# Optimization experiments

Hardware: AMD Instinct MI355X
Metric: run time of the kernel (lower is better)

The kernel has to match this reference:

```python
import jax, jax.numpy as jnp
import numpy as np

B, N_IN, D_IN = 2048, 49, 320
D = 768            # inner_dim
H = 8              # n_heads
DH = D // H        # head dim = 96
NQ = 8             # n_queries
D_OUT = 3072       # llama_hidden
EPS = 1e-5


def _ln(x, g, b):
    mu = jnp.mean(x, axis=-1, keepdims=True)
    var = jnp.mean(jnp.square(x - mu), axis=-1, keepdims=True)
    return (x - mu) * jax.lax.rsqrt(var + EPS) * g + b


def setup_inputs() -> dict:
    key = jax.random.key(0)
    ks = jax.random.split(key, 16)
    s = lambda k, shape, fan: jax.random.normal(k, shape, jnp.float32) * (1.0 / np.sqrt(fan))
    return {
        "features": jax.random.normal(ks[0], (B, N_IN, D_IN), jnp.float32),
        "input_proj_w": s(ks[1], (D, D_IN), D_IN),
        "input_proj_b": jnp.zeros((D,), jnp.float32),
        "queries": jax.random.normal(ks[2], (NQ, D), jnp.float32) * 0.02,
        "ln_q_g": jnp.ones((D,), jnp.float32), "ln_q_b": jnp.zeros((D,), jnp.float32),
        "ln_kv_g": jnp.ones((D,), jnp.float32), "ln_kv_b": jnp.zeros((D,), jnp.float32),
        "in_proj_w": s(ks[3], (3 * D, D), D),
        "in_proj_b": jnp.zeros((3 * D,), jnp.float32),
        "out_proj_w": s(ks[4], (D, D), D),
        "out_proj_b": jnp.zeros((D,), jnp.float32),
        "ln_ff_g": jnp.ones((D,), jnp.float32), "ln_ff_b": jnp.zeros((D,), jnp.float32),
        "ffn_w1": s(ks[5], (D, D), D), "ffn_b1": jnp.zeros((D,), jnp.float32),
        "ffn_w2": s(ks[6], (D, D), D), "ffn_b2": jnp.zeros((D,), jnp.float32),
        "output_proj_w": s(ks[7], (D_OUT, D), D),
        "output_proj_b": jnp.zeros((D_OUT,), jnp.float32),
        "final_g": jnp.ones((D_OUT,), jnp.float32), "final_b": jnp.zeros((D_OUT,), jnp.float32),
    }


def reference(features, input_proj_w, input_proj_b, queries,
              ln_q_g, ln_q_b, ln_kv_g, ln_kv_b,
              in_proj_w, in_proj_b, out_proj_w, out_proj_b,
              ln_ff_g, ln_ff_b, ffn_w1, ffn_b1, ffn_w2, ffn_b2,
              output_proj_w, output_proj_b, final_g, final_b):
    b = features.shape[0]
    # kv projection: (B, N_in, D)
    kv = jnp.einsum('bnd,ed->bne', features, input_proj_w) + input_proj_b
    q = jnp.broadcast_to(queries[None], (b, NQ, D))

    # --- single layer (n_layers=1) ---
    q_norm = _ln(q, ln_q_g, ln_q_b)
    kv_norm = _ln(kv, ln_kv_g, ln_kv_b)

    wq, wk, wv = in_proj_w[:D], in_proj_w[D:2 * D], in_proj_w[2 * D:]
    bq, bk, bv = in_proj_b[:D], in_proj_b[D:2 * D], in_proj_b[2 * D:]
    qp = (jnp.einsum('bqd,ed->bqe', q_norm, wq) + bq).reshape(b, NQ, H, DH)
    kp = (jnp.einsum('bnd,ed->bne', kv_norm, wk) + bk).reshape(b, N_IN, H, DH)
    vp = (jnp.einsum('bnd,ed->bne', kv_norm, wv) + bv).reshape(b, N_IN, H, DH)

    scores = jnp.einsum('bqhd,bnhd->bhqn', qp, kp) / np.sqrt(DH).astype(np.float32)
    attn = jax.nn.softmax(scores, axis=-1)
    ctx = jnp.einsum('bhqn,bnhd->bqhd', attn, vp).reshape(b, NQ, D)
    attn_out = jnp.einsum('bqd,ed->bqe', ctx, out_proj_w) + out_proj_b

    q = q + attn_out
    h = _ln(q, ln_ff_g, ln_ff_b)
    h = jnp.einsum('bqd,ed->bqe', h, ffn_w1) + ffn_b1
    h = jax.nn.gelu(h, approximate=False)
    h = jnp.einsum('bqd,ed->bqe', h, ffn_w2) + ffn_b2
    q = q + h

    out = jnp.einsum('bqd,ed->bqe', q, output_proj_w) + output_proj_b
    return _ln(out, final_g, final_b)
```

## Files before the change

kernel.cpp:

```cpp
#include <hip/hip_runtime.h>
#include <math.h>

typedef __attribute__((ext_vector_type(8))) short short8;
typedef __attribute__((ext_vector_type(8))) unsigned short ushort8;
typedef __attribute__((ext_vector_type(4))) float f32x4;

__device__ __forceinline__ float b2f(unsigned short h) {
    union { unsigned int u; float f; } c; c.u = ((unsigned int)h) << 16; return c.f;
}
__device__ __forceinline__ unsigned short f2b(float x) {
    union { float f; unsigned int u; } c; c.f = x;
    unsigned int r = c.u + 0x7fffu + ((c.u >> 16) & 1u);
    return (unsigned short)(r >> 16);
}

__global__ __launch_bounds__(256) void cast_f2b(const float* __restrict__ in,
                                                unsigned short* __restrict__ out, int n4) {
    int i = blockIdx.x * 256 + threadIdx.x;
    if (i >= n4) return;
    float4 f = ((const float4*)in)[i];
    ushort4 o; o.x = f2b(f.x); o.y = f2b(f.y); o.z = f2b(f.z); o.w = f2b(f.w);
    ((ushort4*)out)[i] = o;
}

template <int DD, bool INB, bool OUTB>
__global__ __launch_bounds__(256) void ln_rows(const void* __restrict__ in_, void* __restrict__ out_,
                                               const float* __restrict__ g, const float* __restrict__ bb,
                                               int nrows) {
    const int wv = threadIdx.x >> 6, l = threadIdx.x & 63;
    const int row = blockIdx.x * 4 + wv;
    if (row >= nrows) return;
    constexpr int NC = DD / 256;
    float v[DD / 64];
    if constexpr (INB) {
        const ushort4* in = (const ushort4*)((const unsigned short*)in_ + (size_t)row * DD);
#pragma unroll
        for (int c = 0; c < NC; ++c) {
            ushort4 u = in[l + 64 * c];
            v[4*c] = b2f(u.x); v[4*c+1] = b2f(u.y); v[4*c+2] = b2f(u.z); v[4*c+3] = b2f(u.w);
        }
    } else {
        const float4* in = (const float4*)((const float*)in_ + (size_t)row * DD);
#pragma unroll
        for (int c = 0; c < NC; ++c) {
            float4 u = in[l + 64 * c];
            v[4*c] = u.x; v[4*c+1] = u.y; v[4*c+2] = u.z; v[4*c+3] = u.w;
        }
    }
    float s = 0.f, s2 = 0.f;
#pragma unroll
    for (int i = 0; i < DD / 64; ++i) { s += v[i]; s2 += v[i] * v[i]; }
#pragma unroll
    for (int o = 32; o > 0; o >>= 1) { s += __shfl_xor(s, o, 64); s2 += __shfl_xor(s2, o, 64); }
    const float mu = s * (1.0f / DD);
    const float var = s2 * (1.0f / DD) - mu * mu;
    const float rs = rsqrtf(var + 1e-5f);
    if constexpr (OUTB) {
        ushort4* out = (ushort4*)((unsigned short*)out_ + (size_t)row * DD);
#pragma unroll
        for (int c = 0; c < NC; ++c) {
            int e = (l + 64 * c) * 4;
            ushort4 o4;
            o4.x = f2b((v[4*c]   - mu) * rs * g[e]   + bb[e]);
            o4.y = f2b((v[4*c+1] - mu) * rs * g[e+1] + bb[e+1]);
            o4.z = f2b((v[4*c+2] - mu) * rs * g[e+2] + bb[e+2]);
            o4.w = f2b((v[4*c+3] - mu) * rs * g[e+3] + bb[e+3]);
            out[l + 64 * c] = o4;
        }
    } else {
        float4* out = (float4*)((float*)out_ + (size_t)row * DD);
#pragma unroll
        for (int c = 0; c < NC; ++c) {
            int e = (l + 64 * c) * 4;
            float4 o4;
            o4.x = (v[4*c]   - mu) * rs * g[e]   + bb[e];
            o4.y = (v[4*c+1] - mu) * rs * g[e+1] + bb[e+1];
            o4.z = (v[4*c+2] - mu) * rs * g[e+2] + bb[e+2];
            o4.w = (v[4*c+3] - mu) * rs * g[e+3] + bb[e+3];
            out[l + 64 * c] = o4;
        }
    }
}

__global__ __launch_bounds__(256) void qp_kernel(const float* __restrict__ qn, const float* __restrict__ wq,
                                                 const float* __restrict__ bq, float* __restrict__ qp) {
    int q = blockIdx.x / 3;
    int col = (blockIdx.x % 3) * 256 + threadIdx.x;
    const float4* a = (const float4*)(qn + q * 768);
    const float4* wr = (const float4*)(wq + (size_t)col * 768);
    float s = 0.f;
#pragma unroll 8
    for (int k = 0; k < 192; ++k) {
        float4 xx = a[k], yy = wr[k];
        s += xx.x * yy.x + xx.y * yy.y + xx.z * yy.z + xx.w * yy.w;
    }
    qp[q * 768 + col] = s + bq[col];
}

__global__ __launch_bounds__(256) void qk_build(const float* __restrict__ qp, const float* __restrict__ wk,
                                                unsigned short* __restrict__ qk) {
    const int hq = blockIdx.x, h = hq >> 3, q = hq & 7;
    const float* qv = qp + q * 768 + h * 96;
#pragma unroll
    for (int c = 0; c < 3; ++c) {
        int e = threadIdx.x + 256 * c;
        float s = 0.f;
        for (int d = 0; d < 96; ++d) s += qv[d] * wk[(size_t)(h * 96 + d) * 768 + e];
        qk[hq * 768 + e] = f2b(s * 0.10206207262f);
    }
}

__device__ __forceinline__ void gll16(const void* g, void* l) {
    __builtin_amdgcn_global_load_lds((const __attribute__((address_space(1))) unsigned int*)g,
                                     (__attribute__((address_space(3))) unsigned int*)l, 16, 0, 0);
}

template <int ROWS>
__device__ __forceinline__ void stage_rows(const unsigned short* gbase, int ldg,
                                           unsigned short* lds, int tid) {
    int wuni = tid & ~63;
#pragma unroll
    for (int it = 0; it < ROWS / 32; ++it) {
        int s = it * 256 + tid;
        int r = s >> 3, c = s & 7;
        int cc = c ^ (r & 7);
        gll16(gbase + (size_t)r * ldg + cc * 8, lds + (size_t)(it * 256 + wuni) * 8);
    }
}

template <int EPI>
__global__ __launch_bounds__(256) void gemm_bf16(
    const unsigned short* __restrict__ A, const unsigned short* __restrict__ W,
    const float* __restrict__ bias, void* __restrict__ out,
    const float* __restrict__ aux, int K, int N) {
    __shared__ __align__(16) unsigned short lA[128 * 64];
    __shared__ __align__(16) unsigned short lB[128 * 64];
    const int tid = threadIdx.x;
    const int l = tid & 63, w = tid >> 6;
    int gx = gridDim.x;
    int lid = blockIdx.y * gx + blockIdx.x;
    int nwg = gx * gridDim.y;
    int idx = (nwg & 7) ? lid : ((lid & 7) * (nwg >> 3) + (lid >> 3));
    const int bm0 = (idx / gx) * 128, bn0 = (idx % gx) * 128;
    const int wm = (w >> 1) * 64, wn = (w & 1) * 64;
    const int l15 = l & 15, lk = l >> 4;
    f32x4 acc[4][4] = {};
    const int nk = K >> 6;
    const unsigned short* Abase = A + (size_t)bm0 * K;
    const unsigned short* Wbase = W + (size_t)bn0 * K;
    for (int kt = 0; kt < nk; ++kt) {
        stage_rows<128>(Abase + kt * 64, K, lA, tid);
        stage_rows<128>(Wbase + kt * 64, K, lB, tid);
        __syncthreads();
        short8 af[4], bf[4];
#pragma unroll
        for (int kk = 0; kk < 2; ++kk) {
#pragma unroll
            for (int mf = 0; mf < 4; ++mf) {
                int r = wm + mf * 16 + l15;
                int c = (kk * 4 + lk) ^ (r & 7);
                af[mf] = *(const short8*)(lA + r * 64 + c * 8);
            }
#pragma unroll
            for (int nf = 0; nf < 4; ++nf) {
                int r = wn + nf * 16 + l15;
                int c = (kk * 4 + lk) ^ (r & 7);
                bf[nf] = *(const short8*)(lB + r * 64 + c * 8);
            }
#pragma unroll
            for (int mf = 0; mf < 4; ++mf)
#pragma unroll
                for (int nf = 0; nf < 4; ++nf)
                    acc[mf][nf] = __builtin_amdgcn_mfma_f32_16x16x32_bf16(af[mf], bf[nf], acc[mf][nf], 0, 0, 0);
        }
        __syncthreads();
    }
    const int row0 = bm0 + wm + (lk << 2);
    const int col0 = bn0 + wn + l15;
#pragma unroll
    for (int nf = 0; nf < 4; ++nf) {
        int col = col0 + nf * 16;
        float bv = bias[col];
#pragma unroll
        for (int mf = 0; mf < 4; ++mf) {
#pragma unroll
            for (int r = 0; r < 4; ++r) {
                int row = row0 + mf * 16 + r;
                float v = acc[mf][nf][r] + bv;
                size_t idx2 = (size_t)row * N + col;
                if constexpr (EPI == 0) {
                    ((unsigned short*)out)[idx2] = f2b(v);
                } else if constexpr (EPI == 1) {
                    v += aux[(row & 7) * N + col];
                    ((float*)out)[idx2] = v;
                } else if constexpr (EPI == 2) {
                    v = 0.5f * v * (1.0f + erff(v * 0.70710678118f));
                    ((unsigned short*)out)[idx2] = f2b(v);
                } else if constexpr (EPI == 3) {
                    v += aux[idx2];
                    ((unsigned short*)out)[idx2] = f2b(v);
                } else {
                    ((float*)out)[idx2] = v;
                }
            }
        }
    }
}

__global__ __launch_bounds__(256) void gemm_scores(const unsigned short* __restrict__ A,
                                                   const unsigned short* __restrict__ Qk,
                                                   float* __restrict__ S) {
    __shared__ __align__(16) unsigned short lA[128 * 64];
    __shared__ __align__(16) unsigned short lB[64 * 64];
    const int tid = threadIdx.x;
    const int l = tid & 63, w = tid >> 6;
    int lid = blockIdx.x;
    int idx = (lid & 7) * (gridDim.x >> 3) + (lid >> 3);
    const int bm0 = idx * 128;
    const int wm = (w >> 1) * 64, wn = (w & 1) * 32;
    const int l15 = l & 15, lk = l >> 4;
    f32x4 acc[4][2] = {};
    const unsigned short* Abase = A + (size_t)bm0 * 768;
    for (int kt = 0; kt < 12; ++kt) {
        stage_rows<128>(Abase + kt * 64, 768, lA, tid);
        stage_rows<64>(Qk + kt * 64, 768, lB, tid);
        __syncthreads();
        short8 af[4], bf[2];
#pragma unroll
        for (int kk = 0; kk < 2; ++kk) {
#pragma unroll
            for (int mf = 0; mf < 4; ++mf) {
                int r = wm + mf * 16 + l15;
                int c = (kk * 4 + lk) ^ (r & 7);
                af[mf] = *(const short8*)(lA + r * 64 + c * 8);
            }
#pragma unroll
            for (int nf = 0; nf < 2; ++nf) {
                int r = wn + nf * 16 + l15;
                int c = (kk * 4 + lk) ^ (r & 7);
                bf[nf] = *(const short8*)(lB + r * 64 + c * 8);
            }
#pragma unroll
            for (int mf = 0; mf < 4; ++mf)
#pragma unroll
                for (int nf = 0; nf < 2; ++nf)
                    acc[mf][nf] = __builtin_amdgcn_mfma_f32_16x16x32_bf16(af[mf], bf[nf], acc[mf][nf], 0, 0, 0);
        }
        __syncthreads();
    }
    const int row0 = bm0 + wm + (lk << 2);
    const int col0 = wn + l15;
#pragma unroll
    for (int nf = 0; nf < 2; ++nf)
#pragma unroll
        for (int mf = 0; mf < 4; ++mf)
#pragma unroll
            for (int r = 0; r < 4; ++r)
                S[(size_t)(row0 + mf * 16 + r) * 64 + col0 + nf * 16] = acc[mf][nf][r];
}

__global__ __launch_bounds__(256) void attn_mix(const unsigned short* __restrict__ kvn,
                                                const float* __restrict__ S,
                                                unsigned short* __restrict__ cmix) {
    __shared__ __align__(16) unsigned short at[64 * 64];
    __shared__ __align__(16) unsigned short kvT[384 * 64];
    float* Sl = (float*)kvT;
    const int b = blockIdx.x;
    const int t = threadIdx.x, l = t & 63, w = t >> 6;
    const int l15 = l & 15, lk = l >> 4;

    for (int i = t; i < 3136; i += 256) Sl[i] = S[(size_t)b * 3136 + i];
    __syncthreads();
    if (w == 0) {
        float mx = -1e30f;
        for (int n = 0; n < 49; ++n) mx = fmaxf(mx, Sl[n * 64 + l]);
        float sum = 0.f;
        for (int n = 0; n < 49; ++n) sum += __expf(Sl[n * 64 + l] - mx);
        float inv = 1.0f / sum;
#pragma unroll
        for (int c = 0; c < 8; ++c) {
            int cc = c ^ (l & 7);
            for (int j = 0; j < 8; ++j) {
                int n = c * 8 + j;
                float a = (n < 49) ? __expf(Sl[n * 64 + l] - mx) * inv : 0.f;
                at[l * 64 + cc * 8 + j] = f2b(a);
            }
        }
    }
    __syncthreads();

    const unsigned short* src = kvn + ((size_t)b * 49 + (l < 49 ? l : 0)) * 768;
#pragma unroll 1
    for (int half = 0; half < 2; ++half) {
        for (int i = 0; i < 12; ++i) {
            int e0 = w * 8 + i * 32;
            ushort8 v = {0, 0, 0, 0, 0, 0, 0, 0};
            if (l < 49) v = *(const ushort8*)(src + half * 384 + e0);
#pragma unroll
            for (int j = 0; j < 8; ++j) {
                int e = e0 + j;
                kvT[e * 64 + (((l >> 3) ^ (e & 7)) << 3) + (l & 7)] = v[j];
            }
        }
        __syncthreads();
#pragma unroll 1
        for (int c2 = 0; c2 < 2; ++c2) {
            int ebase = w * 96 + c2 * 48;
            f32x4 acc[4][3] = {};
#pragma unroll
            for (int ks = 0; ks < 2; ++ks) {
                short8 af[4], bf[3];
#pragma unroll
                for (int mf = 0; mf < 4; ++mf) {
                    int r = mf * 16 + l15;
                    af[mf] = *(const short8*)(at + r * 64 + (((ks * 4 + lk) ^ (r & 7)) << 3));
                }
#pragma unroll
                for (int nf = 0; nf < 3; ++nf) {
                    int er = ebase + nf * 16 + l15;
                    bf[nf] = *(const short8*)(kvT + er * 64 + (((ks * 4 + lk) ^ (er & 7)) << 3));
                }
#pragma unroll
                for (int mf = 0; mf < 4; ++mf)
#pragma unroll
                    for (int nf = 0; nf < 3; ++nf)
                        acc[mf][nf] = __builtin_amdgcn_mfma_f32_16x16x32_bf16(af[mf], bf[nf], acc[mf][nf], 0, 0, 0);
            }
#pragma unroll
            for (int mf = 0; mf < 4; ++mf)
#pragma unroll
                for (int nf = 0; nf < 3; ++nf)
#pragma unroll
                    for (int r = 0; r < 4; ++r) {
                        int hq = mf * 16 + lk * 4 + r;
                        int e = half * 384 + ebase + nf * 16 + l15;
                        cmix[((size_t)(hq >> 3) * 16384 + b * 8 + (hq & 7)) * 768 + e] = f2b(acc[mf][nf][r]);
                    }
        }
        __syncthreads();
    }
}

__global__ __launch_bounds__(256) void gemm_ctx(const unsigned short* __restrict__ cmix,
                                                const unsigned short* __restrict__ wvb,
                                                const float* __restrict__ bv,
                                                unsigned short* __restrict__ ctx) {
    __shared__ __align__(16) unsigned short lA[128 * 64];
    __shared__ __align__(16) unsigned short lB[128 * 64];
    const int tid = threadIdx.x;
    const int l = tid & 63, w = tid >> 6;
    const int h = blockIdx.z;
    int yy = blockIdx.y;
    int idx = (yy & 7) * 16 + (yy >> 3);
    const int bm0 = idx * 128;
    const int wm = (w >> 1) * 64, wn = (w & 1) * 64;
    const int l15 = l & 15, lk = l >> 4;
    f32x4 acc[4][4] = {};
    const unsigned short* Abase = cmix + (size_t)h * 16384 * 768 + (size_t)bm0 * 768;
    const unsigned short* Wbase = wvb + (size_t)h * 96 * 768;
    for (int kt = 0; kt < 12; ++kt) {
        stage_rows<128>(Abase + kt * 64, 768, lA, tid);
        stage_rows<128>(Wbase + kt * 64, 768, lB, tid);
        __syncthreads();
        short8 af[4], bf[4];
#pragma unroll
        for (int kk = 0; kk < 2; ++kk) {
#pragma unroll
            for (int mf = 0; mf < 4; ++mf) {
                int r = wm + mf * 16 + l15;
                int c = (kk * 4 + lk) ^ (r & 7);
                af[mf] = *(const short8*)(lA + r * 64 + c * 8);
            }
#pragma unroll
            for (int nf = 0; nf < 4; ++nf) {
                int r = wn + nf * 16 + l15;
                int c = (kk * 4 + lk) ^ (r & 7);
                bf[nf] = *(const short8*)(lB + r * 64 + c * 8);
            }
#pragma unroll
            for (int mf = 0; mf < 4; ++mf)
#pragma unroll
                for (int nf = 0; nf < 4; ++nf)
                    acc[mf][nf] = __builtin_amdgcn_mfma_f32_16x16x32_bf16(af[mf], bf[nf], acc[mf][nf], 0, 0, 0);
        }
        __syncthreads();
    }
    const int row0 = bm0 + wm + (lk << 2);
    const int col0 = wn + l15;
#pragma unroll
    for (int nf = 0; nf < 4; ++nf) {
        int col = col0 + nf * 16;
        if (col >= 96) continue;
        float bvv = bv[h * 96 + col];
#pragma unroll
        for (int mf = 0; mf < 4; ++mf)
#pragma unroll
            for (int r = 0; r < 4; ++r) {
                int row = row0 + mf * 16 + r;
                ctx[(size_t)row * 768 + h * 96 + col] = f2b(acc[mf][nf][r] + bvv);
            }
    }
}

extern "C" void kernel_launch(void* const* d_in, const int* in_sizes, int n_in,
                              void* d_out, int out_size, void* d_ws, size_t ws_size,
                              hipStream_t stream) {
    (void)in_sizes; (void)n_in; (void)out_size;
    const float* features      = (const float*)d_in[0];
    const float* input_proj_w  = (const float*)d_in[1];
    const float* input_proj_b  = (const float*)d_in[2];
    const float* queries       = (const float*)d_in[3];
    const float* ln_q_g        = (const float*)d_in[4];
    const float* ln_q_b        = (const float*)d_in[5];
    const float* ln_kv_g       = (const float*)d_in[6];
    const float* ln_kv_b       = (const float*)d_in[7];
    const float* in_proj_w     = (const float*)d_in[8];
    const float* in_proj_b     = (const float*)d_in[9];
    const float* out_proj_w    = (const float*)d_in[10];
    const float* out_proj_b    = (const float*)d_in[11];
    const float* ln_ff_g       = (const float*)d_in[12];
    const float* ln_ff_b       = (const float*)d_in[13];
    const float* ffn_w1        = (const float*)d_in[14];
    const float* ffn_b1        = (const float*)d_in[15];
    const float* ffn_w2        = (const float*)d_in[16];
    const float* ffn_b2        = (const float*)d_in[17];
    const float* output_proj_w = (const float*)d_in[18];
    const float* output_proj_b = (const float*)d_in[19];
    const float* final_g       = (const float*)d_in[20];
    const float* final_b       = (const float*)d_in[21];

    char* ws = (char*)d_ws;
    size_t off = 0;
    auto alloc = [&](size_t bytes) -> char* {
        char* r = ws + off; off += (bytes + 255) & ~(size_t)255; return r;
    };
    unsigned short* featb = (unsigned short*)alloc(100352ull * 320 * 2);
    unsigned short* kvbuf = (unsigned short*)alloc(100352ull * 768 * 2);
    unsigned short* cmix  = (unsigned short*)alloc(8ull * 16384 * 768 * 2);
    float*          S     = (float*)alloc(100352ull * 64 * 4);
    unsigned short* winb  = (unsigned short*)alloc(768ull * 320 * 2);
    unsigned short* wvb   = (unsigned short*)alloc(768ull * 768 * 2);
    unsigned short* woutb = (unsigned short*)alloc(768ull * 768 * 2);
    unsigned short* w1b   = (unsigned short*)alloc(768ull * 768 * 2);
    unsigned short* w2b   = (unsigned short*)alloc(768ull * 768 * 2);
    unsigned short* wopb  = (unsigned short*)alloc(3072ull * 768 * 2);
    float* qnorm          = (float*)alloc(8 * 768 * 4);
    float* qpb            = (float*)alloc(8 * 768 * 4);
    unsigned short* qkb   = (unsigned short*)alloc(64ull * 768 * 2);
    if (off > ws_size) return;

    unsigned short* ctx = featb;
    float* x            = (float*)cmix;
    unsigned short* hn  = (unsigned short*)((char*)cmix + 50331648);
    unsigned short* f1  = (unsigned short*)((char*)cmix + 75497472);
    unsigned short* x2  = (unsigned short*)((char*)cmix + 100663296);

    cast_f2b<<<31360, 256, 0, stream>>>(features, featb, 8028160);
    cast_f2b<<<240,   256, 0, stream>>>(input_proj_w, winb, 61440);
    cast_f2b<<<576,   256, 0, stream>>>(in_proj_w + 2 * 768 * 768, wvb, 147456);
    cast_f2b<<<576,   256, 0, stream>>>(out_proj_w, woutb, 147456);
    cast_f2b<<<576,   256, 0, stream>>>(ffn_w1, w1b, 147456);
    cast_f2b<<<576,   256, 0, stream>>>(ffn_w2, w2b, 147456);
    cast_f2b<<<2304,  256, 0, stream>>>(output_proj_w, wopb, 589824);

    ln_rows<768, false, false><<<2, 256, 0, stream>>>(queries, qnorm, ln_q_g, ln_q_b, 8);
    qp_kernel<<<24, 256, 0, stream>>>(qnorm, in_proj_w, in_proj_b, qpb);
    qk_build<<<64, 256, 0, stream>>>(qpb, in_proj_w + 768 * 768, qkb);

    gemm_bf16<0><<<dim3(6, 784), 256, 0, stream>>>(featb, winb, input_proj_b, kvbuf, nullptr, 320, 768);
    ln_rows<768, true, true><<<25088, 256, 0, stream>>>(kvbuf, kvbuf, ln_kv_g, ln_kv_b, 100352);
    gemm_scores<<<784, 256, 0, stream>>>(kvbuf, qkb, S);
    attn_mix<<<2048, 256, 0, stream>>>(kvbuf, S, cmix);
    gemm_ctx<<<dim3(1, 128, 8), 256, 0, stream>>>(cmix, wvb, in_proj_b + 1536, ctx);
    gemm_bf16<1><<<dim3(6, 128), 256, 0, stream>>>(ctx, woutb, out_proj_b, x, queries, 768, 768);
    ln_rows<768, false, true><<<4096, 256, 0, stream>>>(x, hn, ln_ff_g, ln_ff_b, 16384);
    gemm_bf16<2><<<dim3(6, 128), 256, 0, stream>>>(hn, w1b, ffn_b1, f1, nullptr, 768, 768);
    gemm_bf16<3><<<dim3(6, 128), 256, 0, stream>>>(f1, w2b, ffn_b2, x2, x, 768, 768);
    gemm_bf16<4><<<dim3(24, 128), 256, 0, stream>>>(x2, wopb, output_proj_b, d_out, nullptr, 768, 3072);
    ln_rows<3072, false, false><<<4096, 256, 0, stream>>>((float*)d_out, (float*)d_out, final_g, final_b, 16384);
}
```

Measured before the change: 816.5 us.

## Fold kv LayerNorm algebraically into scores and attention mixing; bf16 output proj

Replaces the in-place kv LayerNorm pass with a stats-only kernel that computes per-row rstd and mean. The gamma scaling is folded into the precomputed query-key matrix, with a column correction term, so scores come from raw kv. The mean/rstd correction and the gamma/beta affine are applied inside attn_mix using softmax-weighted stats. It also writes the output projection as bf16 into a scratch buffer before the final LayerNorm instead of fp32 to d_out, cutting write and read traffic. The risks are extra precision loss from single-pass variance and from bf16 rounding of the pre-LN output.

```diff
diff --git a/kernel.cpp b/kernel.cpp
--- a/kernel.cpp
+++ b/kernel.cpp
@@ -82,6 +82,28 @@
     }
 }
 
+__global__ __launch_bounds__(256) void ln_stats(const unsigned short* __restrict__ kv,
+                                                float2* __restrict__ stats, int nrows) {
+    const int wv = threadIdx.x >> 6, l = threadIdx.x & 63;
+    const int row = blockIdx.x * 4 + wv;
+    if (row >= nrows) return;
+    const ushort4* in = (const ushort4*)(kv + (size_t)row * 768);
+    float s = 0.f, s2 = 0.f;
+#pragma unroll
+    for (int c = 0; c < 3; ++c) {
+        ushort4 u = in[l + 64 * c];
+        float a = b2f(u.x), b = b2f(u.y), cc = b2f(u.z), d = b2f(u.w);
+        s += a + b + cc + d;
+        s2 += a * a + b * b + cc * cc + d * d;
+    }
+#pragma unroll
+    for (int o = 32; o > 0; o >>= 1) { s += __shfl_xor(s, o, 64); s2 += __shfl_xor(s2, o, 64); }
+    const float mu = s * (1.0f / 768.0f);
+    const float var = s2 * (1.0f / 768.0f) - mu * mu;
+    const float rs = rsqrtf(var + 1e-5f);
+    if (l == 0) stats[row] = make_float2(rs, rs * mu);
+}
+
 __global__ __launch_bounds__(256) void qp_kernel(const float* __restrict__ qn, const float* __restrict__ wq,
                                                  const float* __restrict__ bq, float* __restrict__ qp) {
     int q = blockIdx.x / 3;
@@ -98,16 +120,27 @@
 }
 
 __global__ __launch_bounds__(256) void qk_build(const float* __restrict__ qp, const float* __restrict__ wk,
-                                                unsigned short* __restrict__ qk) {
+                                                const float* __restrict__ g,
+                                                unsigned short* __restrict__ qkg, float* __restrict__ tout) {
+    __shared__ float red[4];
     const int hq = blockIdx.x, h = hq >> 3, q = hq & 7;
+    const int tid = threadIdx.x;
     const float* qv = qp + q * 768 + h * 96;
+    float tsum = 0.f;
 #pragma unroll
     for (int c = 0; c < 3; ++c) {
-        int e = threadIdx.x + 256 * c;
+        int e = tid + 256 * c;
         float s = 0.f;
         for (int d = 0; d < 96; ++d) s += qv[d] * wk[(size_t)(h * 96 + d) * 768 + e];
-        qk[hq * 768 + e] = f2b(s * 0.10206207262f);
-    }
+        unsigned short bv = f2b(s * 0.10206207262f * g[e]);
+        qkg[hq * 768 + e] = bv;
+        tsum += b2f(bv);
+    }
+#pragma unroll
+    for (int o = 32; o > 0; o >>= 1) tsum += __shfl_xor(tsum, o, 64);
+    if ((tid & 63) == 0) red[tid >> 6] = tsum;
+    __syncthreads();
+    if (tid == 0) tout[hq] = red[0] + red[1] + red[2] + red[3];
 }
 
 __device__ __forceinline__ void gll16(const void* g, void* l) {
@@ -209,6 +242,8 @@
 
 __global__ __launch_bounds__(256) void gemm_scores(const unsigned short* __restrict__ A,
                                                    const unsigned short* __restrict__ Qk,
+                                                   const float2* __restrict__ stats,
+                                                   const float* __restrict__ tcol,
                                                    float* __restrict__ S) {
     __shared__ __align__(16) unsigned short lA[128 * 64];
     __shared__ __align__(16) unsigned short lB[64 * 64];
@@ -250,20 +285,27 @@
     }
     const int row0 = bm0 + wm + (lk << 2);
     const int col0 = wn + l15;
-#pragma unroll
-    for (int nf = 0; nf < 2; ++nf)
-#pragma unroll
-        for (int mf = 0; mf < 4; ++mf)
-#pragma unroll
-            for (int r = 0; r < 4; ++r)
-                S[(size_t)(row0 + mf * 16 + r) * 64 + col0 + nf * 16] = acc[mf][nf][r];
-}
-
-__global__ __launch_bounds__(256) void attn_mix(const unsigned short* __restrict__ kvn,
+    const float tv0 = tcol[col0], tv1 = tcol[col0 + 16];
+#pragma unroll
+    for (int mf = 0; mf < 4; ++mf)
+#pragma unroll
+        for (int r = 0; r < 4; ++r) {
+            int row = row0 + mf * 16 + r;
+            float2 st = stats[row];
+            S[(size_t)row * 64 + col0]      = st.x * acc[mf][0][r] - st.y * tv0;
+            S[(size_t)row * 64 + col0 + 16] = st.x * acc[mf][1][r] - st.y * tv1;
+        }
+}
+
+__global__ __launch_bounds__(256) void attn_mix(const unsigned short* __restrict__ kvr,
                                                 const float* __restrict__ S,
+                                                const float2* __restrict__ stats,
+                                                const float* __restrict__ lg,
+                                                const float* __restrict__ lb,
                                                 unsigned short* __restrict__ cmix) {
     __shared__ __align__(16) unsigned short at[64 * 64];
     __shared__ __align__(16) unsigned short kvT[384 * 64];
+    __shared__ float dl[64];
     float* Sl = (float*)kvT;
     const int b = blockIdx.x;
     const int t = threadIdx.x, l = t & 63, w = t >> 6;
@@ -277,19 +319,27 @@
         float sum = 0.f;
         for (int n = 0; n < 49; ++n) sum += __expf(Sl[n * 64 + l] - mx);
         float inv = 1.0f / sum;
+        float dacc = 0.f;
 #pragma unroll
         for (int c = 0; c < 8; ++c) {
             int cc = c ^ (l & 7);
             for (int j = 0; j < 8; ++j) {
                 int n = c * 8 + j;
-                float a = (n < 49) ? __expf(Sl[n * 64 + l] - mx) * inv : 0.f;
-                at[l * 64 + cc * 8 + j] = f2b(a);
-            }
-        }
+                float av = 0.f;
+                if (n < 49) {
+                    float a = __expf(Sl[n * 64 + l] - mx) * inv;
+                    float2 st = stats[(size_t)b * 49 + n];
+                    av = a * st.x;
+                    dacc += a * st.y;
+                }
+                at[l * 64 + cc * 8 + j] = f2b(av);
+            }
+        }
+        dl[l] = dacc;
     }
     __syncthreads();
 
-    const unsigned short* src = kvn + ((size_t)b * 49 + (l < 49 ? l : 0)) * 768;
+    const unsigned short* src = kvr + ((size_t)b * 49 + (l < 49 ? l : 0)) * 768;
 #pragma unroll 1
     for (int half = 0; half < 2; ++half) {
         for (int i = 0; i < 12; ++i) {
@@ -327,15 +377,18 @@
                         acc[mf][nf] = __builtin_amdgcn_mfma_f32_16x16x32_bf16(af[mf], bf[nf], acc[mf][nf], 0, 0, 0);
             }
 #pragma unroll
-            for (int mf = 0; mf < 4; ++mf)
-#pragma unroll
-                for (int nf = 0; nf < 3; ++nf)
+            for (int nf = 0; nf < 3; ++nf) {
+                int e = half * 384 + ebase + nf * 16 + l15;
+                float gg = lg[e], bbv = lb[e];
+#pragma unroll
+                for (int mf = 0; mf < 4; ++mf)
 #pragma unroll
                     for (int r = 0; r < 4; ++r) {
                         int hq = mf * 16 + lk * 4 + r;
-                        int e = half * 384 + ebase + nf * 16 + l15;
-                        cmix[((size_t)(hq >> 3) * 16384 + b * 8 + (hq & 7)) * 768 + e] = f2b(acc[mf][nf][r]);
+                        float val = gg * (acc[mf][nf][r] - dl[hq]) + bbv;
+                        cmix[((size_t)(hq >> 3) * 16384 + b * 8 + (hq & 7)) * 768 + e] = f2b(val);
                     }
+            }
         }
         __syncthreads();
     }
@@ -438,6 +491,7 @@
     unsigned short* kvbuf = (unsigned short*)alloc(100352ull * 768 * 2);
     unsigned short* cmix  = (unsigned short*)alloc(8ull * 16384 * 768 * 2);
     float*          S     = (float*)alloc(100352ull * 64 * 4);
+    float2*         stats = (float2*)alloc(100352ull * 8);
     unsigned short* winb  = (unsigned short*)alloc(768ull * 320 * 2);
     unsigned short* wvb   = (unsigned short*)alloc(768ull * 768 * 2);
     unsigned short* woutb = (unsigned short*)alloc(768ull * 768 * 2);
@@ -447,13 +501,15 @@
     float* qnorm          = (float*)alloc(8 * 768 * 4);
     float* qpb            = (float*)alloc(8 * 768 * 4);
     unsigned short* qkb   = (unsigned short*)alloc(64ull * 768 * 2);
+    float* tbuf           = (float*)alloc(64 * 4);
     if (off > ws_size) return;
 
-    unsigned short* ctx = featb;
-    float* x            = (float*)cmix;
-    unsigned short* hn  = (unsigned short*)((char*)cmix + 50331648);
-    unsigned short* f1  = (unsigned short*)((char*)cmix + 75497472);
-    unsigned short* x2  = (unsigned short*)((char*)cmix + 100663296);
+    unsigned short* ctx  = featb;
+    unsigned short* outb = kvbuf;
+    float* x             = (float*)cmix;
+    unsigned short* hn   = (unsigned short*)((char*)cmix + 50331648);
+    unsigned short* f1   = (unsigned short*)((char*)cmix + 75497472);
+    unsigned short* x2   = (unsigned short*)((char*)cmix + 100663296);
 
     cast_f2b<<<31360, 256, 0, stream>>>(features, featb, 8028160);
     cast_f2b<<<240,   256, 0, stream>>>(input_proj_w, winb, 61440);
@@ -465,17 +521,17 @@
 
     ln_rows<768, false, false><<<2, 256, 0, stream>>>(queries, qnorm, ln_q_g, ln_q_b, 8);
     qp_kernel<<<24, 256, 0, stream>>>(qnorm, in_proj_w, in_proj_b, qpb);
-    qk_build<<<64, 256, 0, stream>>>(qpb, in_proj_w + 768 * 768, qkb);
+    qk_build<<<64, 256, 0, stream>>>(qpb, in_proj_w + 768 * 768, ln_kv_g, qkb, tbuf);
 
     gemm_bf16<0><<<dim3(6, 784), 256, 0, stream>>>(featb, winb, input_proj_b, kvbuf, nullptr, 320, 768);
-    ln_rows<768, true, true><<<25088, 256, 0, stream>>>(kvbuf, kvbuf, ln_kv_g, ln_kv_b, 100352);
-    gemm_scores<<<784, 256, 0, stream>>>(kvbuf, qkb, S);
-    attn_mix<<<2048, 256, 0, stream>>>(kvbuf, S, cmix);
+    ln_stats<<<25088, 256, 0, stream>>>(kvbuf, stats, 100352);
+    gemm_scores<<<784, 256, 0, stream>>>(kvbuf, qkb, stats, tbuf, S);
+    attn_mix<<<2048, 256, 0, stream>>>(kvbuf, S, stats, ln_kv_g, ln_kv_b, cmix);
     gemm_ctx<<<dim3(1, 128, 8), 256, 0, stream>>>(cmix, wvb, in_proj_b + 1536, ctx);
     gemm_bf16<1><<<dim3(6, 128), 256, 0, stream>>>(ctx, woutb, out_proj_b, x, queries, 768, 768);
     ln_rows<768, false, true><<<4096, 256, 0, stream>>>(x, hn, ln_ff_g, ln_ff_b, 16384);
     gemm_bf16<2><<<dim3(6, 128), 256, 0, stream>>>(hn, w1b, ffn_b1, f1, nullptr, 768, 768);
     gemm_bf16<3><<<dim3(6, 128), 256, 0, stream>>>(f1, w2b, ffn_b2, x2, x, 768, 768);
-    gemm_bf16<4><<<dim3(24, 128), 256, 0, stream>>>(x2, wopb, output_proj_b, d_out, nullptr, 768, 3072);
-    ln_rows<3072, false, false><<<4096, 256, 0, stream>>>((float*)d_out, (float*)d_out, final_g, final_b, 16384);
-}
+    gemm_bf16<0><<<dim3(24, 128), 256, 0, stream>>>(x2, wopb, output_proj_b, outb, nullptr, 768, 3072);
+    ln_rows<3072, true, false><<<4096, 256, 0, stream>>>(outb, (float*)d_out, final_g, final_b, 16384);
+}
```

Result: faster. 776.3 us (-4.9%).
